# Optimization experiments

Hardware: AMD Instinct MI355X
Metric: run time of the kernel (lower is better)

The kernel has to match this reference:

```python
import jax, jax.numpy as jnp
import numpy as np

B, N, D = 2, 4096, 512   # batch, tokens (64x64 latent), query_dim
H, DH = 8, 64            # heads, dim_head; inner_dim = H*DH = 512


def setup_inputs() -> dict:
    key = jax.random.key(0)
    ks = jax.random.split(key, 6)
    s = lambda fan_in: 1.0 / np.sqrt(fan_in)
    x = jax.random.normal(ks[0], (B, N, D), dtype=jnp.float32)
    Wq = jax.random.uniform(ks[1], (D, H * DH), jnp.float32, -s(D), s(D))
    Wk = jax.random.uniform(ks[2], (D, H * DH), jnp.float32, -s(D), s(D))
    Wv = jax.random.uniform(ks[3], (D, H * DH), jnp.float32, -s(D), s(D))
    Wo = jax.random.uniform(ks[4], (H * DH, D), jnp.float32, -s(H * DH), s(H * DH))
    bo = jax.random.uniform(ks[5], (D,), jnp.float32, -s(H * DH), s(H * DH))
    return {"x": x, "Wq": Wq, "Wk": Wk, "Wv": Wv, "Wo": Wo, "bo": bo}


def reference(x, Wq, Wk, Wv, Wo, bo):
    # Self-attention (context = x). Projections (no bias).
    q = x @ Wq  # [B, N, H*DH]
    k = x @ Wk
    v = x @ Wv
    split = lambda t: t.reshape(B, N, H, DH).transpose(0, 2, 1, 3)  # [B, H, N, DH]
    q, k, v = split(q), split(k), split(v)
    scale = DH ** -0.5
    # fp32 upcast for scores (ATTN_PRECISION == 'fp32' path)
    sim = jnp.einsum('bhid,bhjd->bhij', q.astype(jnp.float32), k.astype(jnp.float32)) * scale
    attn = jax.nn.softmax(sim, axis=-1).astype(v.dtype)
    out = jnp.einsum('bhij,bhjd->bhid', attn, v)           # [B, H, N, DH]
    out = out.transpose(0, 2, 1, 3).reshape(B, N, H * DH)  # [B, N, H*DH]
    return out @ Wo + bo  # to_out Linear (dropout=0)
```

## Files before the change

kernel.cpp:

```cpp
#include <hip/hip_runtime.h>
#include <hip/hip_bf16.h>
#include <stdint.h>


typedef short short8 __attribute__((ext_vector_type(8)));
typedef float f32x4 __attribute__((ext_vector_type(4)));
typedef float f32x16 __attribute__((ext_vector_type(16)));

#define QK_SCALE 0.18033688011112042f

static __device__ __forceinline__ unsigned short f32_to_bf16(float f) {
    union { float f; uint32_t u; } v; v.f = f;
    uint32_t u = v.u;
    u += 0x7FFFu + ((u >> 16) & 1u);
    return (unsigned short)(u >> 16);
}

static __device__ __forceinline__ uint32_t cvt_pk_bf16(float lo, float hi) {
    uint32_t r;
    asm("v_cvt_pk_bf16_f32 %0, %1, %2" : "=v"(r) : "v"(lo), "v"(hi));
    return r;
}

static __device__ __forceinline__ int swz(int row, int byte_in_row) {
    return row * 128 + (byte_in_row ^ ((row & 7) << 4));
}

static __device__ __forceinline__ void gload16(const void* g, void* l) {
    __builtin_amdgcn_global_load_lds(
        (const __attribute__((address_space(1))) unsigned int*)g,
        (__attribute__((address_space(3))) unsigned int*)l, 16, 0, 0);
}

union PAU { uint32_t d[4]; short8 v; };

__global__ __launch_bounds__(256) void convert_weights(
    const float* __restrict__ Wq, const float* __restrict__ Wk,
    const float* __restrict__ Wv, const float* __restrict__ Wo,
    unsigned short* __restrict__ wt)
{
    __shared__ float lds[64][65];
    const int mat = blockIdx.z;
    const float* W = (mat == 0) ? Wq : (mat == 1) ? Wk : (mat == 2) ? Wv : Wo;
    const float scale = (mat == 0) ? QK_SCALE : 1.0f;
    unsigned short* out = wt + (size_t)mat * 512 * 512;
    const int k0 = blockIdx.y * 64, n0 = blockIdx.x * 64;
    for (int i = 0; i < 16; i++) {
        int idx = threadIdx.x + i * 256;
        int kl = idx >> 6, nl = idx & 63;
        lds[kl][nl] = W[(size_t)(k0 + kl) * 512 + n0 + nl];
    }
    __syncthreads();
    for (int i = 0; i < 16; i++) {
        int idx = threadIdx.x + i * 256;
        int nr = idx >> 6, kc = idx & 63;
        out[(size_t)(n0 + nr) * 512 + k0 + kc] = f32_to_bf16(lds[kc][nr] * scale);
    }
}

__global__ __launch_bounds__(256) void convert_x(
    const float* __restrict__ x, unsigned short* __restrict__ xbf)
{
    const int idx = (blockIdx.x * 256 + threadIdx.x) * 8;
    float4 f0 = *reinterpret_cast<const float4*>(x + idx);
    float4 f1 = *reinterpret_cast<const float4*>(x + idx + 4);
    short8 v;
    v[0] = (short)f32_to_bf16(f0.x); v[1] = (short)f32_to_bf16(f0.y);
    v[2] = (short)f32_to_bf16(f0.z); v[3] = (short)f32_to_bf16(f0.w);
    v[4] = (short)f32_to_bf16(f1.x); v[5] = (short)f32_to_bf16(f1.y);
    v[6] = (short)f32_to_bf16(f1.z); v[7] = (short)f32_to_bf16(f1.w);
    *reinterpret_cast<short8*>(xbf + idx) = v;
}

__global__ __launch_bounds__(256, 2) void proj_gemm(
    const unsigned short* __restrict__ xbf,
    const unsigned short* __restrict__ wt,
    unsigned short* __restrict__ q_ws,
    unsigned short* __restrict__ k_ws,
    unsigned short* __restrict__ vt_ws)
{
    __shared__ __attribute__((aligned(16))) char smem[65536];
    const int which = blockIdx.z;
    const unsigned short* W = wt + (size_t)which * 512 * 512;
    const int m0 = blockIdx.y * 128, n0 = blockIdx.x * 128;
    const int tid = threadIdx.x, lane = tid & 63, wid = tid >> 6;
    const int wm = (wid >> 1) * 64, wn = (wid & 1) * 64;
    const int rsub = lane >> 3;
    const int cb = ((lane & 7) ^ rsub) << 4;

    f32x4 acc[4][4];
#pragma unroll
    for (int i = 0; i < 4; i++)
#pragma unroll
        for (int j = 0; j < 4; j++) acc[i][j] = (f32x4){0.f, 0.f, 0.f, 0.f};

#define PSTAGE(KT, BUF)                                                           \
    {                                                                             \
        const int kk0_ = (KT) * 64;                                               \
        _Pragma("unroll")                                                         \
        for (int cj = 0; cj < 4; cj++) {                                          \
            const int chunk = wid * 4 + cj;                                       \
            const int row = chunk * 8 + rsub;                                     \
            gload16((const char*)xbf + ((size_t)(m0 + row) * 512 + kk0_) * 2 + cb,\
                    smem + (BUF) * 32768 + chunk * 1024);                         \
            gload16((const char*)W + ((size_t)(n0 + row) * 512 + kk0_) * 2 + cb,  \
                    smem + (BUF) * 32768 + 16384 + chunk * 1024);                 \
        }                                                                         \
    }

    PSTAGE(0, 0);
    __syncthreads();

    for (int kt = 0; kt < 8; kt++) {
        const int cur = kt & 1;
        if (kt + 1 < 8) PSTAGE(kt + 1, cur ^ 1);
        unsigned short* ldsA = (unsigned short*)(smem + cur * 32768);
        unsigned short* ldsB = ldsA + 8192;
#pragma unroll
        for (int ks = 0; ks < 2; ks++) {
            const int kb = ks * 64 + (lane >> 4) * 16;
            short8 a[4], b[4];
#pragma unroll
            for (int m = 0; m < 4; m++)
                a[m] = *reinterpret_cast<short8*>(ldsA + (swz(wm + m * 16 + (lane & 15), kb) >> 1));
#pragma unroll
            for (int n = 0; n < 4; n++)
                b[n] = *reinterpret_cast<short8*>(ldsB + (swz(wn + n * 16 + (lane & 15), kb) >> 1));
            __builtin_amdgcn_s_setprio(1);
#pragma unroll
            for (int m = 0; m < 4; m++)
#pragma unroll
                for (int n = 0; n < 4; n++)
                    acc[m][n] = __builtin_amdgcn_mfma_f32_16x16x32_bf16(a[m], b[n], acc[m][n], 0, 0, 0);
            __builtin_amdgcn_s_setprio(0);
        }
        __syncthreads();
    }
#pragma unroll
    for (int m = 0; m < 4; m++)
#pragma unroll
        for (int n = 0; n < 4; n++)
#pragma unroll
            for (int r = 0; r < 4; r++) {
                int mr = m0 + wm + m * 16 + (lane >> 4) * 4 + r;
                int nc = n0 + wn + n * 16 + (lane & 15);
                unsigned short hv = f32_to_bf16(acc[m][n][r]);
                int b = mr >> 12, tok = mr & 4095;
                int h = nc >> 6, d = nc & 63;
                size_t bh = (size_t)(b * 8 + h);
                if (which == 2) {
                    vt_ws[(bh * 64 + d) * 4096 + tok] = hv;
                } else {
                    unsigned short* dst = (which == 0) ? q_ws : k_ws;
                    dst[(bh * 4096 + tok) * 64 + d] = hv;
                }
            }
}

static __device__ __forceinline__ void pack_pa(const f32x16* p, short8* pa)
{
#pragma unroll
    for (int tt = 0; tt < 2; tt++) {
        uint32_t w0 = cvt_pk_bf16(p[tt][0],  p[tt][1]);
        uint32_t w1 = cvt_pk_bf16(p[tt][2],  p[tt][3]);
        uint32_t w2 = cvt_pk_bf16(p[tt][4],  p[tt][5]);
        uint32_t w3 = cvt_pk_bf16(p[tt][6],  p[tt][7]);
        uint32_t w4 = cvt_pk_bf16(p[tt][8],  p[tt][9]);
        uint32_t w5 = cvt_pk_bf16(p[tt][10], p[tt][11]);
        uint32_t w6 = cvt_pk_bf16(p[tt][12], p[tt][13]);
        uint32_t w7 = cvt_pk_bf16(p[tt][14], p[tt][15]);
        auto r02 = __builtin_amdgcn_permlane32_swap(w0, w2, false, false);
        auto r13 = __builtin_amdgcn_permlane32_swap(w1, w3, false, false);
        auto r46 = __builtin_amdgcn_permlane32_swap(w4, w6, false, false);
        auto r57 = __builtin_amdgcn_permlane32_swap(w5, w7, false, false);
        PAU ua, ub;
        ua.d[0] = r02[0]; ua.d[1] = r13[0]; ua.d[2] = r02[1]; ua.d[3] = r13[1];
        ub.d[0] = r46[0]; ub.d[1] = r57[0]; ub.d[2] = r46[1]; ub.d[3] = r57[1];
        pa[2 * tt]     = ua.v;
        pa[2 * tt + 1] = ub.v;
    }
}

static __device__ __forceinline__ void merge_store(
    f32x16 a0, f32x16 a1, float l_part, int eoff,
    char* smem, int q0, int sw, int g, int lane, int bh,
    unsigned short* __restrict__ o_ws)
{
    const int lo = lane & 31, hi = lane >> 5;
    float* accbuf = (float*)smem;
    float* lbuf   = (float*)(smem + 32768);
    __syncthreads();
    if (g == 0) {
        float* ab = accbuf + sw * 2048;
#pragma unroll
        for (int r = 0; r < 16; r++) {
            int d0 = (r & 3) + 8 * (r >> 2) + 4 * hi;
            ab[d0 * 32 + lo] = a0[r];
            ab[(d0 + 32) * 32 + lo] = a1[r];
        }
        if (hi == 0) lbuf[sw * 32 + lo] = l_part;
    }
    __syncthreads();
    if (g == 1) {
        float rl = __builtin_amdgcn_rcpf(lbuf[sw * 32 + lo] + l_part);
        const float* ab = accbuf + sw * 2048;
        char* eb = smem + 33792 + sw * 4096;
#pragma unroll
        for (int r = 0; r < 16; r++) {
            int d0 = (r & 3) + 8 * (r >> 2) + 4 * hi;
            float o0 = (ab[d0 * 32 + lo] + a0[r]) * rl;
            float o1 = (ab[(d0 + 32) * 32 + lo] + a1[r]) * rl;
            *(unsigned short*)(eb + swz(lo, d0 * 2)) = f32_to_bf16(o0);
            *(unsigned short*)(eb + swz(lo, (d0 + 32) * 2)) = f32_to_bf16(o1);
        }
        const int b = bh >> 3, h = bh & 7;
#pragma unroll
        for (int j = 0; j < 4; j++) {
            int c = lane + 64 * j;
            int row = c >> 3, cc = c & 7;
            short8 v = *reinterpret_cast<short8*>(eb + swz(row, cc * 16));
            int tok = q0 + sw * 64 + eoff + row;
            *reinterpret_cast<short8*>(o_ws + ((size_t)(b * 4096 + tok)) * 512 + h * 64 + cc * 8) = v;
        }
    }
}

__global__ __launch_bounds__(512, 2) void attn_kernel(
    const unsigned short* __restrict__ q_ws,
    const unsigned short* __restrict__ k_ws,
    const unsigned short* __restrict__ vt_ws,
    unsigned short* __restrict__ o_ws)
{
    __shared__ __attribute__((aligned(16))) char smem[65536];
    const int blk = blockIdx.x;
    const int bh = (blk & 7) * 2 + (blk >> 7);
    const int q0 = ((blk >> 3) & 15) * 256;
    const int tid = threadIdx.x, lane = tid & 63, wid = tid >> 6;
    const int g = wid >> 2, sw = wid & 3;
    const int lo = lane & 31, hi = lane >> 5;
    const unsigned short* Qb = q_ws + (size_t)bh * 4096 * 64;
    const unsigned short* Kb = k_ws + (size_t)bh * 4096 * 64 + (size_t)g * 2048 * 64;
    const unsigned short* Vb = vt_ws + (size_t)bh * 64 * 4096 + g * 2048;

    char* gbase = smem + g * 32768;

    short8 qfA[4], qfB[4];
    const int qrA = q0 + sw * 64 + lo;
#pragma unroll
    for (int s = 0; s < 4; s++) {
        qfA[s] = *reinterpret_cast<const short8*>(Qb + (size_t)qrA * 64 + s * 16 + hi * 8);
        qfB[s] = *reinterpret_cast<const short8*>(Qb + (size_t)(qrA + 32) * 64 + s * 16 + hi * 8);
    }

    short8 onesf;
    {
        unsigned short ov = (lo == 0) ? (unsigned short)0x3F80 : (unsigned short)0;
#pragma unroll
        for (int i = 0; i < 8; i++) onesf[i] = (short)ov;
    }

    f32x16 zv;
#pragma unroll
    for (int i = 0; i < 16; i++) zv[i] = 0.f;
    f32x16 accA[2], accB[2], sumA, sumB;
    accA[0] = zv; accA[1] = zv; accB[0] = zv; accB[1] = zv;
    sumA = zv; sumB = zv;

    const int rsub = lane >> 3;
    const int cb = ((lane & 7) ^ rsub) << 4;

#define STAGE(TT, BUF)                                                          \
    {                                                                           \
        const int kv0_ = (TT) * 64;                                             \
        _Pragma("unroll")                                                       \
        for (int j = 0; j < 2; j++) {                                           \
            const int chunk = sw * 2 + j;                                       \
            const int row0 = chunk * 8;                                         \
            gload16((const char*)Kb + (size_t)(kv0_ + row0 + rsub) * 128 + cb,  \
                    gbase + (BUF) * 16384 + chunk * 1024);                      \
            gload16((const char*)Vb + (size_t)(row0 + rsub) * 8192 +            \
                        (size_t)kv0_ * 2 + cb,                                  \
                    gbase + (BUF) * 16384 + 8192 + chunk * 1024);               \
        }                                                                       \
    }

    STAGE(0, 0);
    __syncthreads();

    for (int t = 0; t < 32; t++) {
        const int cur = t & 1;
        if (t + 1 < 32) STAGE(t + 1, cur ^ 1);
        unsigned short* ldsK = (unsigned short*)(gbase + cur * 16384);
        unsigned short* ldsV = ldsK + 4096;

        f32x16 pA[2], pB[2];
        pA[0] = zv; pA[1] = zv; pB[0] = zv; pB[1] = zv;
        __builtin_amdgcn_s_setprio(1);
#pragma unroll
        for (int tt = 0; tt < 2; tt++)
#pragma unroll
            for (int s = 0; s < 4; s++) {
                short8 kf = *reinterpret_cast<short8*>(&ldsK[swz(tt * 32 + lo, s * 32 + hi * 16) >> 1]);
                pA[tt] = __builtin_amdgcn_mfma_f32_32x32x16_bf16(kf, qfA[s], pA[tt], 0, 0, 0);
                pB[tt] = __builtin_amdgcn_mfma_f32_32x32x16_bf16(kf, qfB[s], pB[tt], 0, 0, 0);
            }
        __builtin_amdgcn_s_setprio(0);

#pragma unroll
        for (int tt = 0; tt < 2; tt++)
#pragma unroll
            for (int i = 0; i < 16; i++) {
                pA[tt][i] = __builtin_amdgcn_exp2f(pA[tt][i]);
                pB[tt][i] = __builtin_amdgcn_exp2f(pB[tt][i]);
            }

        short8 paA[4], paB[4];
        pack_pa(pA, paA);
        pack_pa(pB, paB);

        __builtin_amdgcn_s_setprio(1);
#pragma unroll
        for (int dt = 0; dt < 2; dt++)
#pragma unroll
            for (int s = 0; s < 4; s++) {
                short8 vf = *reinterpret_cast<short8*>(&ldsV[swz(dt * 32 + lo, s * 32 + hi * 16) >> 1]);
                accA[dt] = __builtin_amdgcn_mfma_f32_32x32x16_bf16(vf, paA[s], accA[dt], 0, 0, 0);
                accB[dt] = __builtin_amdgcn_mfma_f32_32x32x16_bf16(vf, paB[s], accB[dt], 0, 0, 0);
            }
#pragma unroll
        for (int s = 0; s < 4; s++) {
            sumA = __builtin_amdgcn_mfma_f32_32x32x16_bf16(onesf, paA[s], sumA, 0, 0, 0);
            sumB = __builtin_amdgcn_mfma_f32_32x32x16_bf16(onesf, paB[s], sumB, 0, 0, 0);
        }
        __builtin_amdgcn_s_setprio(0);

        __syncthreads();
    }

    float lA = sumA[0] + __shfl_xor(sumA[0], 32, 64);
    float lB = sumB[0] + __shfl_xor(sumB[0], 32, 64);

    merge_store(accA[0], accA[1], lA, 0,  smem, q0, sw, g, lane, bh, o_ws);
    merge_store(accB[0], accB[1], lB, 32, smem, q0, sw, g, lane, bh, o_ws);
}

__global__ __launch_bounds__(256, 2) void out_gemm(
    const unsigned short* __restrict__ o_ws,
    const unsigned short* __restrict__ wot,
    const float* __restrict__ bo,
    float* __restrict__ out)
{
    __shared__ __attribute__((aligned(16))) char smem[65536];
    const int m0 = blockIdx.y * 128, n0 = blockIdx.x * 128;
    const int tid = threadIdx.x, lane = tid & 63, wid = tid >> 6;
    const int wm = (wid >> 1) * 64, wn = (wid & 1) * 64;
    const int rsub = lane >> 3;
    const int cb = ((lane & 7) ^ rsub) << 4;

    f32x4 acc[4][4];
#pragma unroll
    for (int i = 0; i < 4; i++)
#pragma unroll
        for (int j = 0; j < 4; j++) acc[i][j] = (f32x4){0.f, 0.f, 0.f, 0.f};

#define OSTAGE(KT, BUF)                                                            \
    {                                                                              \
        const int kk0_ = (KT) * 64;                                                \
        _Pragma("unroll")                                                          \
        for (int cj = 0; cj < 4; cj++) {                                           \
            const int chunk = wid * 4 + cj;                                        \
            const int row = chunk * 8 + rsub;                                      \
            gload16((const char*)o_ws + ((size_t)(m0 + row) * 512 + kk0_) * 2 + cb,\
                    smem + (BUF) * 32768 + chunk * 1024);                          \
            gload16((const char*)wot + ((size_t)(n0 + row) * 512 + kk0_) * 2 + cb, \
                    smem + (BUF) * 32768 + 16384 + chunk * 1024);                  \
        }                                                                          \
    }

    OSTAGE(0, 0);
    __syncthreads();

    for (int kt = 0; kt < 8; kt++) {
        const int cur = kt & 1;
        if (kt + 1 < 8) OSTAGE(kt + 1, cur ^ 1);
        unsigned short* ldsA = (unsigned short*)(smem + cur * 32768);
        unsigned short* ldsB = ldsA + 8192;
#pragma unroll
        for (int ks = 0; ks < 2; ks++) {
            const int kb = ks * 64 + (lane >> 4) * 16;
            short8 a[4], b[4];
#pragma unroll
            for (int m = 0; m < 4; m++)
                a[m] = *reinterpret_cast<short8*>(ldsA + (swz(wm + m * 16 + (lane & 15), kb) >> 1));
#pragma unroll
            for (int n = 0; n < 4; n++)
                b[n] = *reinterpret_cast<short8*>(ldsB + (swz(wn + n * 16 + (lane & 15), kb) >> 1));
            __builtin_amdgcn_s_setprio(1);
#pragma unroll
            for (int m = 0; m < 4; m++)
#pragma unroll
                for (int n = 0; n < 4; n++)
                    acc[m][n] = __builtin_amdgcn_mfma_f32_16x16x32_bf16(a[m], b[n], acc[m][n], 0, 0, 0);
            __builtin_amdgcn_s_setprio(0);
        }
        __syncthreads();
    }
#pragma unroll
    for (int n = 0; n < 4; n++) {
        const int nc = n0 + wn + n * 16 + (lane & 15);
        const float bias = bo[nc];
#pragma unroll
        for (int m = 0; m < 4; m++)
#pragma unroll
            for (int r = 0; r < 4; r++) {
                int mr = m0 + wm + m * 16 + (lane >> 4) * 4 + r;
                out[(size_t)mr * 512 + nc] = acc[m][n][r] + bias;
            }
    }
}

extern "C" void kernel_launch(void* const* d_in, const int* in_sizes, int n_in,
                              void* d_out, int out_size, void* d_ws, size_t ws_size,
                              hipStream_t stream)
{
    const float* x  = (const float*)d_in[0];
    const float* Wq = (const float*)d_in[1];
    const float* Wk = (const float*)d_in[2];
    const float* Wv = (const float*)d_in[3];
    const float* Wo = (const float*)d_in[4];
    const float* bo = (const float*)d_in[5];
    float* out = (float*)d_out;

    char* ws = (char*)d_ws;
    unsigned short* wt    = (unsigned short*)(ws);
    unsigned short* q_ws  = (unsigned short*)(ws + (size_t)(2)  * 1024 * 1024);
    unsigned short* k_ws  = (unsigned short*)(ws + (size_t)(10) * 1024 * 1024);
    unsigned short* vt_ws = (unsigned short*)(ws + (size_t)(18) * 1024 * 1024);
    unsigned short* xbf   = (unsigned short*)(ws + (size_t)(26) * 1024 * 1024);
    unsigned short* o_ws  = xbf;

    convert_weights<<<dim3(8, 8, 4), 256, 0, stream>>>(Wq, Wk, Wv, Wo, wt);
    convert_x<<<dim3(2048), 256, 0, stream>>>(x, xbf);
    proj_gemm<<<dim3(4, 64, 3), 256, 0, stream>>>(xbf, wt, q_ws, k_ws, vt_ws);
    attn_kernel<<<dim3(256), 512, 0, stream>>>(q_ws, k_ws, vt_ws, o_ws);
    out_gemm<<<dim3(4, 64), 256, 0, stream>>>(o_ws, wt + (size_t)3 * 512 * 512, bo, out);
}
```

Baseline: 125.2 us.

## Split attention KV halves across blocks with atomic bf16 merge, normalize in out GEMM

Attention now runs as 256-thread blocks that each handle one KV half for a query tile. Each block accumulates its unnormalized output into global memory with packed bf16 atomics, and its row sums into a float array with atomics. This replaces the in-block LDS merge and its barriers. The output GEMM applies the 1/l normalization while staging its A tile, but loses its double-buffered prefetch. The two conversion kernels are merged into one launch, and two memsets are added to zero the accumulators.

```diff
diff --git a/kernel.cpp b/kernel.cpp
--- a/kernel.cpp
+++ b/kernel.cpp
@@ -22,6 +22,11 @@
     return r;
 }
 
+static __device__ __forceinline__ void atomic_pk_bf16(unsigned short* p, uint32_t v) {
+    asm volatile("global_atomic_pk_add_bf16 %0, %1, off"
+                 :: "v"((uint64_t)(uintptr_t)p), "v"(v) : "memory");
+}
+
 static __device__ __forceinline__ int swz(int row, int byte_in_row) {
     return row * 128 + (byte_in_row ^ ((row & 7) << 4));
 }
@@ -34,42 +39,42 @@
 
 union PAU { uint32_t d[4]; short8 v; };
 
-__global__ __launch_bounds__(256) void convert_weights(
+__global__ __launch_bounds__(256) void convert_pre(
+    const float* __restrict__ x,
     const float* __restrict__ Wq, const float* __restrict__ Wk,
     const float* __restrict__ Wv, const float* __restrict__ Wo,
-    unsigned short* __restrict__ wt)
+    unsigned short* __restrict__ wt, unsigned short* __restrict__ xbf)
 {
     __shared__ float lds[64][65];
-    const int mat = blockIdx.z;
-    const float* W = (mat == 0) ? Wq : (mat == 1) ? Wk : (mat == 2) ? Wv : Wo;
-    const float scale = (mat == 0) ? QK_SCALE : 1.0f;
-    unsigned short* out = wt + (size_t)mat * 512 * 512;
-    const int k0 = blockIdx.y * 64, n0 = blockIdx.x * 64;
-    for (int i = 0; i < 16; i++) {
-        int idx = threadIdx.x + i * 256;
-        int kl = idx >> 6, nl = idx & 63;
-        lds[kl][nl] = W[(size_t)(k0 + kl) * 512 + n0 + nl];
-    }
-    __syncthreads();
-    for (int i = 0; i < 16; i++) {
-        int idx = threadIdx.x + i * 256;
-        int nr = idx >> 6, kc = idx & 63;
-        out[(size_t)(n0 + nr) * 512 + k0 + kc] = f32_to_bf16(lds[kc][nr] * scale);
-    }
-}
-
-__global__ __launch_bounds__(256) void convert_x(
-    const float* __restrict__ x, unsigned short* __restrict__ xbf)
-{
-    const int idx = (blockIdx.x * 256 + threadIdx.x) * 8;
-    float4 f0 = *reinterpret_cast<const float4*>(x + idx);
-    float4 f1 = *reinterpret_cast<const float4*>(x + idx + 4);
-    short8 v;
-    v[0] = (short)f32_to_bf16(f0.x); v[1] = (short)f32_to_bf16(f0.y);
-    v[2] = (short)f32_to_bf16(f0.z); v[3] = (short)f32_to_bf16(f0.w);
-    v[4] = (short)f32_to_bf16(f1.x); v[5] = (short)f32_to_bf16(f1.y);
-    v[6] = (short)f32_to_bf16(f1.z); v[7] = (short)f32_to_bf16(f1.w);
-    *reinterpret_cast<short8*>(xbf + idx) = v;
+    const int bx = blockIdx.x;
+    if (bx < 256) {
+        const int mat = bx >> 6, rem = bx & 63;
+        const int k0 = (rem >> 3) * 64, n0 = (rem & 7) * 64;
+        const float* W = (mat == 0) ? Wq : (mat == 1) ? Wk : (mat == 2) ? Wv : Wo;
+        const float scale = (mat == 0) ? QK_SCALE : 1.0f;
+        unsigned short* out = wt + (size_t)mat * 512 * 512;
+        for (int i = 0; i < 16; i++) {
+            int idx = threadIdx.x + i * 256;
+            int kl = idx >> 6, nl = idx & 63;
+            lds[kl][nl] = W[(size_t)(k0 + kl) * 512 + n0 + nl];
+        }
+        __syncthreads();
+        for (int i = 0; i < 16; i++) {
+            int idx = threadIdx.x + i * 256;
+            int nr = idx >> 6, kc = idx & 63;
+            out[(size_t)(n0 + nr) * 512 + k0 + kc] = f32_to_bf16(lds[kc][nr] * scale);
+        }
+    } else {
+        const int idx = ((bx - 256) * 256 + threadIdx.x) * 8;
+        float4 f0 = *reinterpret_cast<const float4*>(x + idx);
+        float4 f1 = *reinterpret_cast<const float4*>(x + idx + 4);
+        short8 v;
+        v[0] = (short)f32_to_bf16(f0.x); v[1] = (short)f32_to_bf16(f0.y);
+        v[2] = (short)f32_to_bf16(f0.z); v[3] = (short)f32_to_bf16(f0.w);
+        v[4] = (short)f32_to_bf16(f1.x); v[5] = (short)f32_to_bf16(f1.y);
+        v[6] = (short)f32_to_bf16(f1.z); v[7] = (short)f32_to_bf16(f1.w);
+        *reinterpret_cast<short8*>(xbf + idx) = v;
+    }
 }
 
 __global__ __launch_bounds__(256, 2) void proj_gemm(
@@ -181,68 +186,23 @@
     }
 }
 
-static __device__ __forceinline__ void merge_store(
-    f32x16 a0, f32x16 a1, float l_part, int eoff,
-    char* smem, int q0, int sw, int g, int lane, int bh,
-    unsigned short* __restrict__ o_ws)
-{
-    const int lo = lane & 31, hi = lane >> 5;
-    float* accbuf = (float*)smem;
-    float* lbuf   = (float*)(smem + 32768);
-    __syncthreads();
-    if (g == 0) {
-        float* ab = accbuf + sw * 2048;
-#pragma unroll
-        for (int r = 0; r < 16; r++) {
-            int d0 = (r & 3) + 8 * (r >> 2) + 4 * hi;
-            ab[d0 * 32 + lo] = a0[r];
-            ab[(d0 + 32) * 32 + lo] = a1[r];
-        }
-        if (hi == 0) lbuf[sw * 32 + lo] = l_part;
-    }
-    __syncthreads();
-    if (g == 1) {
-        float rl = __builtin_amdgcn_rcpf(lbuf[sw * 32 + lo] + l_part);
-        const float* ab = accbuf + sw * 2048;
-        char* eb = smem + 33792 + sw * 4096;
-#pragma unroll
-        for (int r = 0; r < 16; r++) {
-            int d0 = (r & 3) + 8 * (r >> 2) + 4 * hi;
-            float o0 = (ab[d0 * 32 + lo] + a0[r]) * rl;
-            float o1 = (ab[(d0 + 32) * 32 + lo] + a1[r]) * rl;
-            *(unsigned short*)(eb + swz(lo, d0 * 2)) = f32_to_bf16(o0);
-            *(unsigned short*)(eb + swz(lo, (d0 + 32) * 2)) = f32_to_bf16(o1);
-        }
-        const int b = bh >> 3, h = bh & 7;
-#pragma unroll
-        for (int j = 0; j < 4; j++) {
-            int c = lane + 64 * j;
-            int row = c >> 3, cc = c & 7;
-            short8 v = *reinterpret_cast<short8*>(eb + swz(row, cc * 16));
-            int tok = q0 + sw * 64 + eoff + row;
-            *reinterpret_cast<short8*>(o_ws + ((size_t)(b * 4096 + tok)) * 512 + h * 64 + cc * 8) = v;
-        }
-    }
-}
-
-__global__ __launch_bounds__(512, 2) void attn_kernel(
+__global__ __launch_bounds__(256, 2) void attn_kernel(
     const unsigned short* __restrict__ q_ws,
     const unsigned short* __restrict__ k_ws,
     const unsigned short* __restrict__ vt_ws,
-    unsigned short* __restrict__ o_ws)
-{
-    __shared__ __attribute__((aligned(16))) char smem[65536];
+    unsigned short* __restrict__ o_unnorm,
+    float* __restrict__ l_arr)
+{
+    __shared__ __attribute__((aligned(16))) char smem[32768];
     const int blk = blockIdx.x;
-    const int bh = (blk & 7) * 2 + (blk >> 7);
-    const int q0 = ((blk >> 3) & 15) * 256;
-    const int tid = threadIdx.x, lane = tid & 63, wid = tid >> 6;
-    const int g = wid >> 2, sw = wid & 3;
+    const int L = (blk & 7) * 64 + (blk >> 3);
+    const int bh = L >> 5, g = (L >> 4) & 1, qt = L & 15;
+    const int q0 = qt * 256;
+    const int tid = threadIdx.x, lane = tid & 63, sw = tid >> 6;
     const int lo = lane & 31, hi = lane >> 5;
     const unsigned short* Qb = q_ws + (size_t)bh * 4096 * 64;
     const unsigned short* Kb = k_ws + (size_t)bh * 4096 * 64 + (size_t)g * 2048 * 64;
     const unsigned short* Vb = vt_ws + (size_t)bh * 64 * 4096 + g * 2048;
-
-    char* gbase = smem + g * 32768;
 
     short8 qfA[4], qfB[4];
     const int qrA = q0 + sw * 64 + lo;
@@ -277,10 +237,10 @@
             const int chunk = sw * 2 + j;                                       \
             const int row0 = chunk * 8;                                         \
             gload16((const char*)Kb + (size_t)(kv0_ + row0 + rsub) * 128 + cb,  \
-                    gbase + (BUF) * 16384 + chunk * 1024);                      \
+                    smem + (BUF) * 16384 + chunk * 1024);                       \
             gload16((const char*)Vb + (size_t)(row0 + rsub) * 8192 +            \
                         (size_t)kv0_ * 2 + cb,                                  \
-                    gbase + (BUF) * 16384 + 8192 + chunk * 1024);               \
+                    smem + (BUF) * 16384 + 8192 + chunk * 1024);                \
         }                                                                       \
     }
 
@@ -290,7 +250,7 @@
     for (int t = 0; t < 32; t++) {
         const int cur = t & 1;
         if (t + 1 < 32) STAGE(t + 1, cur ^ 1);
-        unsigned short* ldsK = (unsigned short*)(gbase + cur * 16384);
+        unsigned short* ldsK = (unsigned short*)(smem + cur * 16384);
         unsigned short* ldsV = ldsK + 4096;
 
         f32x16 pA[2], pB[2];
@@ -337,25 +297,38 @@
         __syncthreads();
     }
 
-    float lA = sumA[0] + __shfl_xor(sumA[0], 32, 64);
-    float lB = sumB[0] + __shfl_xor(sumB[0], 32, 64);
-
-    merge_store(accA[0], accA[1], lA, 0,  smem, q0, sw, g, lane, bh, o_ws);
-    merge_store(accB[0], accB[1], lB, 32, smem, q0, sw, g, lane, bh, o_ws);
+    const int b = bh >> 3, h = bh & 7;
+    if (hi == 0) {
+        atomicAdd(l_arr + bh * 4096 + qrA, sumA[0]);
+        atomicAdd(l_arr + bh * 4096 + qrA + 32, sumB[0]);
+    }
+    unsigned short* orowA = o_unnorm + ((size_t)(b * 4096 + qrA)) * 512 + h * 64;
+    unsigned short* orowB = orowA + (size_t)32 * 512;
+#pragma unroll
+    for (int dt = 0; dt < 2; dt++)
+#pragma unroll
+        for (int r0 = 0; r0 < 16; r0 += 4) {
+            int d0 = dt * 32 + 8 * (r0 >> 2) + 4 * hi;
+            atomic_pk_bf16(orowA + d0,     cvt_pk_bf16(accA[dt][r0],     accA[dt][r0 + 1]));
+            atomic_pk_bf16(orowA + d0 + 2, cvt_pk_bf16(accA[dt][r0 + 2], accA[dt][r0 + 3]));
+            atomic_pk_bf16(orowB + d0,     cvt_pk_bf16(accB[dt][r0],     accB[dt][r0 + 1]));
+            atomic_pk_bf16(orowB + d0 + 2, cvt_pk_bf16(accB[dt][r0 + 2], accB[dt][r0 + 3]));
+        }
 }
 
 __global__ __launch_bounds__(256, 2) void out_gemm(
-    const unsigned short* __restrict__ o_ws,
+    const unsigned short* __restrict__ o_unnorm,
+    const float* __restrict__ l_arr,
     const unsigned short* __restrict__ wot,
     const float* __restrict__ bo,
     float* __restrict__ out)
 {
-    __shared__ __attribute__((aligned(16))) char smem[65536];
+    __shared__ __attribute__((aligned(16))) char smem[32768];
     const int m0 = blockIdx.y * 128, n0 = blockIdx.x * 128;
     const int tid = threadIdx.x, lane = tid & 63, wid = tid >> 6;
     const int wm = (wid >> 1) * 64, wn = (wid & 1) * 64;
     const int rsub = lane >> 3;
-    const int cb = ((lane & 7) ^ rsub) << 4;
+    const int cbv = ((lane & 7) ^ rsub) << 4;
 
     f32x4 acc[4][4];
 #pragma unroll
@@ -363,47 +336,56 @@
 #pragma unroll
         for (int j = 0; j < 4; j++) acc[i][j] = (f32x4){0.f, 0.f, 0.f, 0.f};
 
-#define OSTAGE(KT, BUF)                                                            \
-    {                                                                              \
-        const int kk0_ = (KT) * 64;                                                \
-        _Pragma("unroll")                                                          \
-        for (int cj = 0; cj < 4; cj++) {                                           \
-            const int chunk = wid * 4 + cj;                                        \
-            const int row = chunk * 8 + rsub;                                      \
-            gload16((const char*)o_ws + ((size_t)(m0 + row) * 512 + kk0_) * 2 + cb,\
-                    smem + (BUF) * 32768 + chunk * 1024);                          \
-            gload16((const char*)wot + ((size_t)(n0 + row) * 512 + kk0_) * 2 + cb, \
-                    smem + (BUF) * 32768 + 16384 + chunk * 1024);                  \
-        }                                                                          \
-    }
-
-    OSTAGE(0, 0);
-    __syncthreads();
+    unsigned short* ldsA = (unsigned short*)smem;
+    unsigned short* ldsB = ldsA + 8192;
 
     for (int kt = 0; kt < 8; kt++) {
-        const int cur = kt & 1;
-        if (kt + 1 < 8) OSTAGE(kt + 1, cur ^ 1);
-        unsigned short* ldsA = (unsigned short*)(smem + cur * 32768);
-        unsigned short* ldsB = ldsA + 8192;
+        const int kk0 = kt * 64;
+        __syncthreads();
+#pragma unroll
+        for (int cj = 0; cj < 4; cj++) {
+            const int chunk = wid * 4 + cj;
+            const int row = chunk * 8 + rsub;
+            gload16((const char*)wot + ((size_t)(n0 + row) * 512 + kk0) * 2 + cbv,
+                    smem + 16384 + chunk * 1024);
+        }
+#pragma unroll
+        for (int i = 0; i < 4; i++) {
+            int c = tid + i * 256;
+            int row = c >> 3, c8 = c & 7;
+            int grow = m0 + row;
+            int b = grow >> 12, tok = grow & 4095;
+            short8 o8 = *reinterpret_cast<const short8*>(
+                o_unnorm + (size_t)grow * 512 + kk0 + c8 * 8);
+            float rl = __builtin_amdgcn_rcpf(l_arr[(size_t)(b * 8 + kt) * 4096 + tok]);
+            short8 a8;
+#pragma unroll
+            for (int j = 0; j < 8; j++) {
+                union { uint32_t u; float f; } cv;
+                cv.u = ((uint32_t)(unsigned short)o8[j]) << 16;
+                a8[j] = (short)f32_to_bf16(cv.f * rl);
+            }
+            *reinterpret_cast<short8*>(ldsA + (swz(row, c8 * 16) >> 1)) = a8;
+        }
+        __syncthreads();
 #pragma unroll
         for (int ks = 0; ks < 2; ks++) {
             const int kb = ks * 64 + (lane >> 4) * 16;
-            short8 a[4], b[4];
+            short8 a[4], bfr[4];
 #pragma unroll
             for (int m = 0; m < 4; m++)
                 a[m] = *reinterpret_cast<short8*>(ldsA + (swz(wm + m * 16 + (lane & 15), kb) >> 1));
 #pragma unroll
             for (int n = 0; n < 4; n++)
-                b[n] = *reinterpret_cast<short8*>(ldsB + (swz(wn + n * 16 + (lane & 15), kb) >> 1));
+                bfr[n] = *reinterpret_cast<short8*>(ldsB + (swz(wn + n * 16 + (lane & 15), kb) >> 1));
             __builtin_amdgcn_s_setprio(1);
 #pragma unroll
             for (int m = 0; m < 4; m++)
 #pragma unroll
                 for (int n = 0; n < 4; n++)
-                    acc[m][n] = __builtin_amdgcn_mfma_f32_16x16x32_bf16(a[m], b[n], acc[m][n], 0, 0, 0);
+                    acc[m][n] = __builtin_amdgcn_mfma_f32_16x16x32_bf16(a[m], bfr[n], acc[m][n], 0, 0, 0);
             __builtin_amdgcn_s_setprio(0);
         }
-        __syncthreads();
     }
 #pragma unroll
     for (int n = 0; n < 4; n++) {
@@ -437,11 +419,13 @@
     unsigned short* k_ws  = (unsigned short*)(ws + (size_t)(10) * 1024 * 1024);
     unsigned short* vt_ws = (unsigned short*)(ws + (size_t)(18) * 1024 * 1024);
     unsigned short* xbf   = (unsigned short*)(ws + (size_t)(26) * 1024 * 1024);
-    unsigned short* o_ws  = xbf;
-
-    convert_weights<<<dim3(8, 8, 4), 256, 0, stream>>>(Wq, Wk, Wv, Wo, wt);
-    convert_x<<<dim3(2048), 256, 0, stream>>>(x, xbf);
+    unsigned short* o_un  = xbf;
+    float*          l_arr = (float*)(ws);
+
+    convert_pre<<<dim3(2304), 256, 0, stream>>>(x, Wq, Wk, Wv, Wo, wt, xbf);
     proj_gemm<<<dim3(4, 64, 3), 256, 0, stream>>>(xbf, wt, q_ws, k_ws, vt_ws);
-    attn_kernel<<<dim3(256), 512, 0, stream>>>(q_ws, k_ws, vt_ws, o_ws);
-    out_gemm<<<dim3(4, 64), 256, 0, stream>>>(o_ws, wt + (size_t)3 * 512 * 512, bo, out);
-}
+    hipMemsetAsync(l_arr, 0, (size_t)16 * 4096 * 4, stream);
+    hipMemsetAsync(o_un, 0, (size_t)8192 * 512 * 2, stream);
+    attn_kernel<<<dim3(512), 256, 0, stream>>>(q_ws, k_ws, vt_ws, o_un, l_arr);
+    out_gemm<<<dim3(4, 64), 256, 0, stream>>>(o_un, l_arr, wt + (size_t)3 * 512 * 512, bo, out);
+}
```

Result: slower. 214.9 us (+71.6%).

## Stagger PV step across wave groups with triple-buffered V and merge convert kernels

Applied to the files above, without the earlier changes.

The attention kernel now triple-buffers V tiles and has the second wave group run the previous iteration's P·V MFMAs before its current QK step, while the first group runs P·V as before. Offsetting the groups this way lets one group's MFMA work overlap the other's exp2 and pack phase. The price is more LDS per block (80 KB instead of 64 KB), which could limit occupancy, plus a tail PV step after the loop. The weight and x conversion kernels are also folded into one launch to remove one kernel launch.

```diff
diff --git a/kernel.cpp b/kernel.cpp
--- a/kernel.cpp
+++ b/kernel.cpp
@@ -34,42 +34,42 @@
 
 union PAU { uint32_t d[4]; short8 v; };
 
-__global__ __launch_bounds__(256) void convert_weights(
+__global__ __launch_bounds__(256) void convert_pre(
+    const float* __restrict__ x,
     const float* __restrict__ Wq, const float* __restrict__ Wk,
     const float* __restrict__ Wv, const float* __restrict__ Wo,
-    unsigned short* __restrict__ wt)
+    unsigned short* __restrict__ wt, unsigned short* __restrict__ xbf)
 {
     __shared__ float lds[64][65];
-    const int mat = blockIdx.z;
-    const float* W = (mat == 0) ? Wq : (mat == 1) ? Wk : (mat == 2) ? Wv : Wo;
-    const float scale = (mat == 0) ? QK_SCALE : 1.0f;
-    unsigned short* out = wt + (size_t)mat * 512 * 512;
-    const int k0 = blockIdx.y * 64, n0 = blockIdx.x * 64;
-    for (int i = 0; i < 16; i++) {
-        int idx = threadIdx.x + i * 256;
-        int kl = idx >> 6, nl = idx & 63;
-        lds[kl][nl] = W[(size_t)(k0 + kl) * 512 + n0 + nl];
-    }
-    __syncthreads();
-    for (int i = 0; i < 16; i++) {
-        int idx = threadIdx.x + i * 256;
-        int nr = idx >> 6, kc = idx & 63;
-        out[(size_t)(n0 + nr) * 512 + k0 + kc] = f32_to_bf16(lds[kc][nr] * scale);
-    }
-}
-
-__global__ __launch_bounds__(256) void convert_x(
-    const float* __restrict__ x, unsigned short* __restrict__ xbf)
-{
-    const int idx = (blockIdx.x * 256 + threadIdx.x) * 8;
-    float4 f0 = *reinterpret_cast<const float4*>(x + idx);
-    float4 f1 = *reinterpret_cast<const float4*>(x + idx + 4);
-    short8 v;
-    v[0] = (short)f32_to_bf16(f0.x); v[1] = (short)f32_to_bf16(f0.y);
-    v[2] = (short)f32_to_bf16(f0.z); v[3] = (short)f32_to_bf16(f0.w);
-    v[4] = (short)f32_to_bf16(f1.x); v[5] = (short)f32_to_bf16(f1.y);
-    v[6] = (short)f32_to_bf16(f1.z); v[7] = (short)f32_to_bf16(f1.w);
-    *reinterpret_cast<short8*>(xbf + idx) = v;
+    const int bx = blockIdx.x;
+    if (bx < 256) {
+        const int mat = bx >> 6, rem = bx & 63;
+        const int k0 = (rem >> 3) * 64, n0 = (rem & 7) * 64;
+        const float* W = (mat == 0) ? Wq : (mat == 1) ? Wk : (mat == 2) ? Wv : Wo;
+        const float scale = (mat == 0) ? QK_SCALE : 1.0f;
+        unsigned short* out = wt + (size_t)mat * 512 * 512;
+        for (int i = 0; i < 16; i++) {
+            int idx = threadIdx.x + i * 256;
+            int kl = idx >> 6, nl = idx & 63;
+            lds[kl][nl] = W[(size_t)(k0 + kl) * 512 + n0 + nl];
+        }
+        __syncthreads();
+        for (int i = 0; i < 16; i++) {
+            int idx = threadIdx.x + i * 256;
+            int nr = idx >> 6, kc = idx & 63;
+            out[(size_t)(n0 + nr) * 512 + k0 + kc] = f32_to_bf16(lds[kc][nr] * scale);
+        }
+    } else {
+        const int idx = ((bx - 256) * 256 + threadIdx.x) * 8;
+        float4 f0 = *reinterpret_cast<const float4*>(x + idx);
+        float4 f1 = *reinterpret_cast<const float4*>(x + idx + 4);
+        short8 v;
+        v[0] = (short)f32_to_bf16(f0.x); v[1] = (short)f32_to_bf16(f0.y);
+        v[2] = (short)f32_to_bf16(f0.z); v[3] = (short)f32_to_bf16(f0.w);
+        v[4] = (short)f32_to_bf16(f1.x); v[5] = (short)f32_to_bf16(f1.y);
+        v[6] = (short)f32_to_bf16(f1.z); v[7] = (short)f32_to_bf16(f1.w);
+        *reinterpret_cast<short8*>(xbf + idx) = v;
+    }
 }
 
 __global__ __launch_bounds__(256, 2) void proj_gemm(
@@ -231,7 +231,7 @@
     const unsigned short* __restrict__ vt_ws,
     unsigned short* __restrict__ o_ws)
 {
-    __shared__ __attribute__((aligned(16))) char smem[65536];
+    __shared__ __attribute__((aligned(16))) char smem[81920];
     const int blk = blockIdx.x;
     const int bh = (blk & 7) * 2 + (blk >> 7);
     const int q0 = ((blk >> 3) & 15) * 256;
@@ -242,7 +242,7 @@
     const unsigned short* Kb = k_ws + (size_t)bh * 4096 * 64 + (size_t)g * 2048 * 64;
     const unsigned short* Vb = vt_ws + (size_t)bh * 64 * 4096 + g * 2048;
 
-    char* gbase = smem + g * 32768;
+    char* gbase = smem + g * 40960;
 
     short8 qfA[4], qfB[4];
     const int qrA = q0 + sw * 64 + lo;
@@ -265,33 +265,59 @@
     f32x16 accA[2], accB[2], sumA, sumB;
     accA[0] = zv; accA[1] = zv; accB[0] = zv; accB[1] = zv;
     sumA = zv; sumB = zv;
+    short8 paA[4], paB[4];
 
     const int rsub = lane >> 3;
     const int cb = ((lane & 7) ^ rsub) << 4;
 
-#define STAGE(TT, BUF)                                                          \
+#define STAGE(TT)                                                               \
     {                                                                           \
         const int kv0_ = (TT) * 64;                                             \
+        char* kdst = gbase + ((TT) & 1) * 8192;                                 \
+        char* vdst = gbase + 16384 + ((TT) % 3) * 8192;                         \
         _Pragma("unroll")                                                       \
         for (int j = 0; j < 2; j++) {                                           \
             const int chunk = sw * 2 + j;                                       \
             const int row0 = chunk * 8;                                         \
             gload16((const char*)Kb + (size_t)(kv0_ + row0 + rsub) * 128 + cb,  \
-                    gbase + (BUF) * 16384 + chunk * 1024);                      \
+                    kdst + chunk * 1024);                                       \
             gload16((const char*)Vb + (size_t)(row0 + rsub) * 8192 +            \
                         (size_t)kv0_ * 2 + cb,                                  \
-                    gbase + (BUF) * 16384 + 8192 + chunk * 1024);               \
+                    vdst + chunk * 1024);                                       \
         }                                                                       \
     }
 
-    STAGE(0, 0);
+#define PVSTEP(LDSV)                                                            \
+    {                                                                           \
+        __builtin_amdgcn_s_setprio(1);                                          \
+        _Pragma("unroll")                                                       \
+        for (int dt = 0; dt < 2; dt++)                                          \
+        _Pragma("unroll")                                                       \
+        for (int s = 0; s < 4; s++) {                                           \
+            short8 vf = *reinterpret_cast<short8*>(&(LDSV)[swz(dt * 32 + lo, s * 32 + hi * 16) >> 1]); \
+            accA[dt] = __builtin_amdgcn_mfma_f32_32x32x16_bf16(vf, paA[s], accA[dt], 0, 0, 0); \
+            accB[dt] = __builtin_amdgcn_mfma_f32_32x32x16_bf16(vf, paB[s], accB[dt], 0, 0, 0); \
+        }                                                                       \
+        _Pragma("unroll")                                                       \
+        for (int s = 0; s < 4; s++) {                                           \
+            sumA = __builtin_amdgcn_mfma_f32_32x32x16_bf16(onesf, paA[s], sumA, 0, 0, 0); \
+            sumB = __builtin_amdgcn_mfma_f32_32x32x16_bf16(onesf, paB[s], sumB, 0, 0, 0); \
+        }                                                                       \
+        __builtin_amdgcn_s_setprio(0);                                          \
+    }
+
+    STAGE(0);
     __syncthreads();
 
+#pragma unroll 1
     for (int t = 0; t < 32; t++) {
-        const int cur = t & 1;
-        if (t + 1 < 32) STAGE(t + 1, cur ^ 1);
-        unsigned short* ldsK = (unsigned short*)(gbase + cur * 16384);
-        unsigned short* ldsV = ldsK + 4096;
+        if (t + 1 < 32) STAGE(t + 1);
+        unsigned short* ldsK = (unsigned short*)(gbase + (t & 1) * 8192);
+
+        if (g == 1 && t > 0) {
+            unsigned short* ldsVp = (unsigned short*)(gbase + 16384 + ((t + 2) % 3) * 8192);
+            PVSTEP(ldsVp);
+        }
 
         f32x16 pA[2], pB[2];
         pA[0] = zv; pA[1] = zv; pB[0] = zv; pB[1] = zv;
@@ -313,28 +339,20 @@
                 pA[tt][i] = __builtin_amdgcn_exp2f(pA[tt][i]);
                 pB[tt][i] = __builtin_amdgcn_exp2f(pB[tt][i]);
             }
-
-        short8 paA[4], paB[4];
         pack_pa(pA, paA);
         pack_pa(pB, paB);
 
-        __builtin_amdgcn_s_setprio(1);
-#pragma unroll
-        for (int dt = 0; dt < 2; dt++)
-#pragma unroll
-            for (int s = 0; s < 4; s++) {
-                short8 vf = *reinterpret_cast<short8*>(&ldsV[swz(dt * 32 + lo, s * 32 + hi * 16) >> 1]);
-                accA[dt] = __builtin_amdgcn_mfma_f32_32x32x16_bf16(vf, paA[s], accA[dt], 0, 0, 0);
-                accB[dt] = __builtin_amdgcn_mfma_f32_32x32x16_bf16(vf, paB[s], accB[dt], 0, 0, 0);
-            }
-#pragma unroll
-        for (int s = 0; s < 4; s++) {
-            sumA = __builtin_amdgcn_mfma_f32_32x32x16_bf16(onesf, paA[s], sumA, 0, 0, 0);
-            sumB = __builtin_amdgcn_mfma_f32_32x32x16_bf16(onesf, paB[s], sumB, 0, 0, 0);
-        }
-        __builtin_amdgcn_s_setprio(0);
+        if (g == 0) {
+            unsigned short* ldsV = (unsigned short*)(gbase + 16384 + (t % 3) * 8192);
+            PVSTEP(ldsV);
+        }
 
         __syncthreads();
+    }
+
+    if (g == 1) {
+        unsigned short* ldsVp = (unsigned short*)(gbase + 16384 + (31 % 3) * 8192);
+        PVSTEP(ldsVp);
     }
 
     float lA = sumA[0] + __shfl_xor(sumA[0], 32, 64);
@@ -439,8 +457,7 @@
     unsigned short* xbf   = (unsigned short*)(ws + (size_t)(26) * 1024 * 1024);
     unsigned short* o_ws  = xbf;
 
-    convert_weights<<<dim3(8, 8, 4), 256, 0, stream>>>(Wq, Wk, Wv, Wo, wt);
-    convert_x<<<dim3(2048), 256, 0, stream>>>(x, xbf);
+    convert_pre<<<dim3(2304), 256, 0, stream>>>(x, Wq, Wk, Wv, Wo, wt, xbf);
     proj_gemm<<<dim3(4, 64, 3), 256, 0, stream>>>(xbf, wt, q_ws, k_ws, vt_ws);
     attn_kernel<<<dim3(256), 512, 0, stream>>>(q_ws, k_ws, vt_ws, o_ws);
     out_gemm<<<dim3(4, 64), 256, 0, stream>>>(o_ws, wt + (size_t)3 * 512 * 512, bo, out);
```

Measured after the change: 125.1 us. About the same (-0.1%).
